# Performance work log

Measured on AMD Instinct MI355X. Metric: run time of the kernel, lower is better.

The kernel has to match this reference:

```python
import jax, jax.numpy as jnp
import numpy as np

BITS = 8
B, S, E = 8, 512, 1024
H = 16
MLP = 4096
LN_EPS = 1e-5


def ste_round(x):
    # straight-through rounding (brevitas round_ste)
    return x + jax.lax.stop_gradient(jnp.round(x) - x)


def fq(x, bits=BITS, signed=True, narrow=False):
    """Per-tensor fake-quant: scale from abs-max stats, round+clamp+rescale."""
    if signed:
        qmax = 2.0 ** (bits - 1) - 1.0
        qmin = -qmax if narrow else -(qmax + 1.0)
        amax = jnp.max(jnp.abs(x))
    else:
        qmax = 2.0 ** bits - 1.0
        qmin = 0.0
        amax = jnp.max(x)
    scale = jnp.maximum(jax.lax.stop_gradient(amax) / qmax, 1e-8)
    return jnp.clip(ste_round(x / scale), qmin, qmax) * scale


def fq_w(w):
    # weight quantizer: 8-bit signed narrow-range, max-stats scale
    return fq(w, bits=8, signed=True, narrow=True)


def layernorm(x, g, b):
    mu = jnp.mean(x, axis=-1, keepdims=True)
    var = jnp.mean(jnp.square(x - mu), axis=-1, keepdims=True)
    return (x - mu) * jax.lax.rsqrt(var + LN_EPS) * g + b


def block_forward(x, Wq, bq, Wk, bk, Wv, bv, Wo, bo, W1, b1, W2, b2, g1, be1, g2, be2):
    Bb, Ss, Ee = x.shape
    D = Ee // H
    # --- quant multihead attention (unpacked in_proj) ---
    q = x @ fq_w(Wq).T + fq(bq, 8)
    k = x @ fq_w(Wk).T + fq(bk, 8)
    v = x @ fq_w(Wv).T + fq(bv, 8)
    qh = q.reshape(Bb, Ss, H, D).transpose(0, 2, 1, 3)   # bhsd
    kh = k.reshape(Bb, Ss, H, D).transpose(0, 2, 1, 3)
    vh = v.reshape(Bb, Ss, H, D).transpose(0, 2, 1, 3)
    q_scaled = fq(qh / jnp.sqrt(jnp.float32(D)))          # q_scaled_quant
    kt = fq(kh)                                            # k_transposed_quant (per-tensor)
    vq = fq(vh)                                            # v_quant
    scores = jnp.einsum('bhqd,bhkd->bhqk', q_scaled, kt)
    scores = fq(scores)                                    # softmax_input_quant
    attn = jax.nn.softmax(scores, axis=-1)
    attn = fq(attn)                                        # attn_output_weights_quant
    ctx = jnp.einsum('bhqk,bhkd->bhqd', attn, vq)
    ctx = ctx.transpose(0, 2, 1, 3).reshape(Bb, Ss, Ee)
    ctx = fq(ctx)                                          # out_proj_input_quant
    sdp_out = ctx @ fq_w(Wo).T + fq(bo, 8)
    # --- residual + norm ---
    h = fq(x) + fq(sdp_out)                                # QuantEltwiseAdd input_quant
    h = fq(layernorm(h, g1, be1))                          # norm_sdp + QuantIdentity
    # --- quant MLP ---
    m = h @ fq_w(W1).T + fq(b1, 8)
    m = fq(jax.nn.relu(m), signed=False)                   # QuantReLU (unsigned)
    m = m @ fq_w(W2).T + fq(b2, 8)
    # --- residual + norm ---
    y = fq(h) + fq(m)
    return fq(layernorm(y, g2, be2))


def setup_inputs() -> dict:
    key = jax.random.key(0)
    ks = jax.random.split(key, 16)
    s_in = 1.0 / np.sqrt(E)
    s_mlp = 1.0 / np.sqrt(MLP)
    return {
        'x': jax.random.normal(ks[0], (B, S, E), jnp.float32),
        'Wq': jax.random.normal(ks[1], (E, E), jnp.float32) * s_in,
        'bq': jax.random.normal(ks[2], (E,), jnp.float32) * 0.01,
        'Wk': jax.random.normal(ks[3], (E, E), jnp.float32) * s_in,
        'bk': jax.random.normal(ks[4], (E,), jnp.float32) * 0.01,
        'Wv': jax.random.normal(ks[5], (E, E), jnp.float32) * s_in,
        'bv': jax.random.normal(ks[6], (E,), jnp.float32) * 0.01,
        'Wo': jax.random.normal(ks[7], (E, E), jnp.float32) * s_in,
        'bo': jax.random.normal(ks[8], (E,), jnp.float32) * 0.01,
        'W1': jax.random.normal(ks[9], (MLP, E), jnp.float32) * s_in,
        'b1': jax.random.normal(ks[10], (MLP,), jnp.float32) * 0.01,
        'W2': jax.random.normal(ks[11], (E, MLP), jnp.float32) * s_mlp,
        'b2': jax.random.normal(ks[12], (E,), jnp.float32) * 0.01,
        'g1': jnp.ones((E,), jnp.float32),
        'be1': jnp.zeros((E,), jnp.float32),
        'g2': jnp.ones((E,), jnp.float32),
        'be2': jnp.zeros((E,), jnp.float32),
    }


def reference(x, Wq, bq, Wk, bk, Wv, bv, Wo, bo, W1, b1, W2, b2, g1, be1, g2, be2):
    return block_forward(x, Wq, bq, Wk, bk, Wv, bv, Wo, bo, W1, b1, W2, b2, g1, be1, g2, be2)
```

## Files before the change

kernel.cpp:

```cpp
#include <hip/hip_runtime.h>
#include <math.h>

#define BB 8
#define SS 512
#define EE 1024
#define HH 16
#define DD 64
#define MLPD 4096
#define NROWS (BB*SS)
#define LNEPS 1e-5f
#define SM_ROWS 8
#define LN_ROWS 8

typedef unsigned short u16;
typedef __attribute__((ext_vector_type(8))) short bf8_t;
typedef __attribute__((ext_vector_type(4))) float f32x4;

enum {
  SL_WQ=0, SL_WK, SL_WV, SL_WO, SL_W1, SL_W2,
  SL_BQ, SL_BK, SL_BV, SL_BO, SL_B1, SL_B2,
  SL_X, SL_Q, SL_K, SL_V, SL_SC, SL_AT, SL_CTX, SL_SDP,
  SL_LN1, SL_M1, SL_M2, SL_LN2, NSLOTS
};

__device__ __forceinline__ void atomicMaxF(float* a, float v) {
  atomicMax((unsigned int*)a, __float_as_uint(v));
}

__device__ __forceinline__ float fqv(float x, float inv, float s, float lo, float hi) {
  return fminf(fmaxf(rintf(x * inv), lo), hi) * s;
}

__device__ __forceinline__ u16 f2bf(float f) {
  unsigned int u = __float_as_uint(f);
  return (u16)((u + 0x7fffu + ((u >> 16) & 1u)) >> 16);
}
__device__ __forceinline__ float bf2f(u16 h) {
  return __uint_as_float((unsigned int)h << 16);
}

__device__ __forceinline__ void gll16(const void* src, void* dst) {
  __builtin_amdgcn_global_load_lds((const __attribute__((address_space(1))) void*)src,
                                   (__attribute__((address_space(3))) void*)dst, 16, 0, 0);
}

__global__ void k_init(float* scal) {
  if (threadIdx.x < NSLOTS) scal[threadIdx.x] = 0.f;
}

__global__ __launch_bounds__(256) void k_amax(const float* __restrict__ p, int n,
                                              float* scal, int slot) {
  float m = 0.f;
  for (int i = blockIdx.x * 256 + threadIdx.x; i < n; i += gridDim.x * 256)
    m = fmaxf(m, fabsf(p[i]));
  #pragma unroll
  for (int o = 32; o > 0; o >>= 1) m = fmaxf(m, __shfl_down(m, o, 64));
  __shared__ float red[4];
  int w = threadIdx.x >> 6;
  if ((threadIdx.x & 63) == 0) red[w] = m;
  __syncthreads();
  if (threadIdx.x == 0) {
    m = fmaxf(fmaxf(red[0], red[1]), fmaxf(red[2], red[3]));
    atomicMaxF(&scal[slot], m);
  }
}

__global__ __launch_bounds__(256) void k_conv_code(const float* __restrict__ in,
    u16* __restrict__ out, long n, const float* __restrict__ scal, int slot,
    float div, float lo, float hi)
{
  const float s = fmaxf(scal[slot] / div, 1e-8f), inv = 1.f / s;
  long i = ((long)blockIdx.x * 256 + threadIdx.x) * 4;
  const long stride = (long)gridDim.x * 1024;
  for (; i < n; i += stride) {
    const float4 v = *(const float4*)&in[i];
    ushort4 o;
    o.x = f2bf(fminf(fmaxf(rintf(v.x * inv), lo), hi));
    o.y = f2bf(fminf(fmaxf(rintf(v.y * inv), lo), hi));
    o.z = f2bf(fminf(fmaxf(rintf(v.z * inv), lo), hi));
    o.w = f2bf(fminf(fmaxf(rintf(v.w * inv), lo), hi));
    *(ushort4*)&out[i] = o;
  }
}

__global__ __launch_bounds__(256) void k_conv_x(const float* __restrict__ in,
    u16* __restrict__ hi, u16* __restrict__ lo, long n)
{
  long i = ((long)blockIdx.x * 256 + threadIdx.x) * 4;
  const long stride = (long)gridDim.x * 1024;
  for (; i < n; i += stride) {
    const float4 v = *(const float4*)&in[i];
    ushort4 h, l;
    h.x = f2bf(v.x); l.x = f2bf(v.x - bf2f(h.x));
    h.y = f2bf(v.y); l.y = f2bf(v.y - bf2f(h.y));
    h.z = f2bf(v.z); l.z = f2bf(v.z - bf2f(h.z));
    h.w = f2bf(v.w); l.w = f2bf(v.w - bf2f(h.w));
    *(ushort4*)&hi[i] = h;
    *(ushort4*)&lo[i] = l;
  }
}

template<bool RAWX>
__global__ __launch_bounds__(256) void k_gemm_mfma(
    const u16* __restrict__ A0, const u16* __restrict__ A1,
    const u16* __restrict__ Bw, const float* __restrict__ bias,
    float* __restrict__ C, int M, int N, int K,
    const float* __restrict__ scal, float* scalw,
    int aslot, float adiv, int bslot, int biasslot, int epi, int epislot)
{
  __shared__ u16 As[128*32];
  __shared__ u16 Al[RAWX ? 128*32 : 16];
  __shared__ u16 Bs[128*32];
  __shared__ float red[4];

  const int t = threadIdx.x;
  const int w = t >> 6, lane = t & 63;
  const int wr = w >> 1, wc = w & 1;
  const int lr = lane & 15, cbl = lane >> 4;
  const int swz = (lr >> 1) & 3;
  const int m0 = blockIdx.y * 128, n0 = blockIdx.x * 128;

  const int srow0 = t >> 2;
  const int scb   = (t & 3) ^ ((srow0 >> 1) & 3);
  const int lo0 = w * 512;
  const int lo1 = 2048 + w * 512;
  const long arow0 = (long)(m0 + srow0)      * K + scb * 8;
  const long arow1 = (long)(m0 + srow0 + 64) * K + scb * 8;
  const long brow0 = (long)(n0 + srow0)      * K + scb * 8;
  const long brow1 = (long)(n0 + srow0 + 64) * K + scb * 8;

  int afo[4], bfo[4];
  #pragma unroll
  for (int i = 0; i < 4; ++i) {
    afo[i] = (wr*64 + i*16 + lr) * 32 + ((cbl ^ swz) * 8);
    bfo[i] = (wc*64 + i*16 + lr) * 32 + ((cbl ^ swz) * 8);
  }

  f32x4 acc[4][4] = {};

  for (int k0 = 0; k0 < K; k0 += 32) {
    gll16(A0 + arow0 + k0, As + lo0);
    gll16(A0 + arow1 + k0, As + lo1);
    if (RAWX) {
      gll16(A1 + arow0 + k0, Al + lo0);
      gll16(A1 + arow1 + k0, Al + lo1);
    }
    gll16(Bw + brow0 + k0, Bs + lo0);
    gll16(Bw + brow1 + k0, Bs + lo1);
    __syncthreads();

    bf8_t afr[4], bfr[4], alo[4];
    #pragma unroll
    for (int i = 0; i < 4; ++i) {
      afr[i] = *(const bf8_t*)&As[afo[i]];
      bfr[i] = *(const bf8_t*)&Bs[bfo[i]];
      if (RAWX) alo[i] = *(const bf8_t*)&Al[afo[i]];
    }
    #pragma unroll
    for (int i = 0; i < 4; ++i)
      #pragma unroll
      for (int j = 0; j < 4; ++j) {
        acc[i][j] = __builtin_amdgcn_mfma_f32_16x16x32_bf16(afr[i], bfr[j], acc[i][j], 0, 0, 0);
        if (RAWX)
          acc[i][j] = __builtin_amdgcn_mfma_f32_16x16x32_bf16(alo[i], bfr[j], acc[i][j], 0, 0, 0);
      }
    __syncthreads();
  }

  float sA = 1.f;
  if (aslot >= 0) sA = fmaxf(scal[aslot] / adiv, 1e-8f);
  const float sB = fmaxf(scal[bslot] / 127.f, 1e-8f);
  const float sAB = sA * sB;
  const float sb = fmaxf(scal[biasslot] / 127.f, 1e-8f), invb = 1.f / sb;

  float em = 0.f;
  #pragma unroll
  for (int j = 0; j < 4; ++j) {
    const int col = n0 + wc*64 + j*16 + lr;
    const float bq = fqv(bias[col], invb, sb, -128.f, 127.f);
    #pragma unroll
    for (int i = 0; i < 4; ++i) {
      const int rowb = m0 + wr*64 + i*16 + cbl*4;
      #pragma unroll
      for (int r = 0; r < 4; ++r) {
        const float c = acc[i][j][r] * sAB + bq;
        C[(long)(rowb + r) * N + col] = c;
        em = (epi == 2) ? fmaxf(em, c) : fmaxf(em, fabsf(c));
      }
    }
  }
  #pragma unroll
  for (int o = 32; o > 0; o >>= 1) em = fmaxf(em, __shfl_down(em, o, 64));
  if ((lane) == 0) red[w] = em;
  __syncthreads();
  if (t == 0)
    atomicMaxF(&scalw[epislot], fmaxf(fmaxf(red[0], red[1]), fmaxf(red[2], red[3])));
}

__global__ __launch_bounds__(256) void k_scores(
    const float* __restrict__ q, const float* __restrict__ kk,
    float* __restrict__ sc, float* scal)
{
  __shared__ float Qs[64][65];
  __shared__ float Ks[64][65];
  __shared__ float red[4];
  const int bz = blockIdx.z, b = bz >> 4, h = bz & 15;
  const int tx = threadIdx.x & 15, ty = threadIdx.x >> 4;
  const int m0 = blockIdx.y * 64, n0 = blockIdx.x * 64;
  const long base = (long)b * SS * EE + h * DD;

  const float sq = fmaxf((scal[SL_Q] * 0.125f) / 127.f, 1e-8f), invq = 1.f / sq;
  const float sk = fmaxf(scal[SL_K] / 127.f, 1e-8f), invk = 1.f / sk;

  #pragma unroll
  for (int p = 0; p < 16; ++p) {
    int e = threadIdx.x + p * 256;
    int r = e >> 6, c = e & 63;
    float qv = q[base + (long)(m0 + r) * EE + c] * 0.125f;
    Qs[c][r] = fqv(qv, invq, sq, -128.f, 127.f);
    float kv = kk[base + (long)(n0 + r) * EE + c];
    Ks[c][r] = fqv(kv, invk, sk, -128.f, 127.f);
  }
  __syncthreads();

  float acc[4][4] = {{0.f}};
  #pragma unroll
  for (int kx = 0; kx < 64; ++kx) {
    float a[4], bv[4];
    #pragma unroll
    for (int i = 0; i < 4; ++i) a[i] = Qs[kx][ty + 16 * i];
    #pragma unroll
    for (int j = 0; j < 4; ++j) bv[j] = Ks[kx][tx + 16 * j];
    #pragma unroll
    for (int i = 0; i < 4; ++i)
      #pragma unroll
      for (int j = 0; j < 4; ++j)
        acc[i][j] += a[i] * bv[j];
  }

  float em = 0.f;
  #pragma unroll
  for (int i = 0; i < 4; ++i)
    #pragma unroll
    for (int j = 0; j < 4; ++j) {
      float c = acc[i][j];
      sc[((long)bz * SS + m0 + ty + 16 * i) * SS + n0 + tx + 16 * j] = c;
      em = fmaxf(em, fabsf(c));
    }
  #pragma unroll
  for (int o = 32; o > 0; o >>= 1) em = fmaxf(em, __shfl_down(em, o, 64));
  int w = threadIdx.x >> 6;
  if ((threadIdx.x & 63) == 0) red[w] = em;
  __syncthreads();
  if (threadIdx.x == 0)
    atomicMaxF(&scal[SL_SC], fmaxf(fmaxf(red[0], red[1]), fmaxf(red[2], red[3])));
}

__global__ __launch_bounds__(256) void k_softmax(float* __restrict__ sc, float* scal) {
  const int w = threadIdx.x >> 6, lane = threadIdx.x & 63;
  const float ss = fmaxf(scal[SL_SC] / 127.f, 1e-8f), inv = 1.f / ss;
  float am = 0.f;
  long row = ((long)blockIdx.x * 4 + w) * SM_ROWS;
  for (int r = 0; r < SM_ROWS; ++r, ++row) {
    float4* p = (float4*)(sc + row * SS);
    float4 a = p[lane];
    float4 b = p[lane + 64];
    float v[8];
    v[0] = fqv(a.x, inv, ss, -128.f, 127.f);
    v[1] = fqv(a.y, inv, ss, -128.f, 127.f);
    v[2] = fqv(a.z, inv, ss, -128.f, 127.f);
    v[3] = fqv(a.w, inv, ss, -128.f, 127.f);
    v[4] = fqv(b.x, inv, ss, -128.f, 127.f);
    v[5] = fqv(b.y, inv, ss, -128.f, 127.f);
    v[6] = fqv(b.z, inv, ss, -128.f, 127.f);
    v[7] = fqv(b.w, inv, ss, -128.f, 127.f);
    float m = v[0];
    #pragma unroll
    for (int i = 1; i < 8; ++i) m = fmaxf(m, v[i]);
    #pragma unroll
    for (int o = 32; o > 0; o >>= 1) m = fmaxf(m, __shfl_xor(m, o, 64));
    float e[8], s = 0.f;
    #pragma unroll
    for (int i = 0; i < 8; ++i) { e[i] = expf(v[i] - m); s += e[i]; }
    #pragma unroll
    for (int o = 32; o > 0; o >>= 1) s += __shfl_xor(s, o, 64);
    const float rinv = 1.f / s;
    a.x = e[0] * rinv; a.y = e[1] * rinv; a.z = e[2] * rinv; a.w = e[3] * rinv;
    b.x = e[4] * rinv; b.y = e[5] * rinv; b.z = e[6] * rinv; b.w = e[7] * rinv;
    p[lane] = a;
    p[lane + 64] = b;
    am = fmaxf(am, rinv);
  }
  __shared__ float red[4];
  if (lane == 0) red[w] = am;
  __syncthreads();
  if (threadIdx.x == 0)
    atomicMaxF(&scal[SL_AT], fmaxf(fmaxf(red[0], red[1]), fmaxf(red[2], red[3])));
}

__global__ __launch_bounds__(256) void k_ctx(
    const float* __restrict__ at, const float* __restrict__ v,
    float* __restrict__ ctx, float* scal)
{
  __shared__ float As[16][65];
  __shared__ float Vs[16][68];
  __shared__ float red[4];
  const int bz = blockIdx.y, b = bz >> 4, h = bz & 15;
  const int tx = threadIdx.x & 15, ty = threadIdx.x >> 4;
  const int m0 = blockIdx.x * 64;
  const long abase = (long)bz * SS * SS;
  const long vbase = (long)b * SS * EE + h * DD;

  const float sa = fmaxf(scal[SL_AT] / 127.f, 1e-8f), inva = 1.f / sa;
  const float sv = fmaxf(scal[SL_V] / 127.f, 1e-8f), invv = 1.f / sv;

  float acc[4][4] = {{0.f}};
  for (int k0 = 0; k0 < SS; k0 += 16) {
    #pragma unroll
    for (int p = 0; p < 4; ++p) {
      int e = threadIdx.x + p * 256;
      int r = e >> 4, c = e & 15;
      float a = at[abase + (long)(m0 + r) * SS + k0 + c];
      As[c][r] = fqv(a, inva, sa, -128.f, 127.f);
    }
    {
      int r = threadIdx.x >> 6, c = threadIdx.x & 63;
      #pragma unroll
      for (int p = 0; p < 4; ++p) {
        int rr = r + p * 4;
        float vv = v[vbase + (long)(k0 + rr) * EE + c];
        Vs[rr][c] = fqv(vv, invv, sv, -128.f, 127.f);
      }
    }
    __syncthreads();
    #pragma unroll
    for (int kx = 0; kx < 16; ++kx) {
      float a[4], bv[4];
      #pragma unroll
      for (int i = 0; i < 4; ++i) a[i] = As[kx][ty + 16 * i];
      #pragma unroll
      for (int j = 0; j < 4; ++j) bv[j] = Vs[kx][tx + 16 * j];
      #pragma unroll
      for (int i = 0; i < 4; ++i)
        #pragma unroll
        for (int j = 0; j < 4; ++j)
          acc[i][j] += a[i] * bv[j];
    }
    __syncthreads();
  }

  float em = 0.f;
  #pragma unroll
  for (int i = 0; i < 4; ++i)
    #pragma unroll
    for (int j = 0; j < 4; ++j) {
      float c = acc[i][j];
      ctx[((long)b * SS + m0 + ty + 16 * i) * EE + h * DD + tx + 16 * j] = c;
      em = fmaxf(em, fabsf(c));
    }
  #pragma unroll
  for (int o = 32; o > 0; o >>= 1) em = fmaxf(em, __shfl_down(em, o, 64));
  int w = threadIdx.x >> 6;
  if ((threadIdx.x & 63) == 0) red[w] = em;
  __syncthreads();
  if (threadIdx.x == 0)
    atomicMaxF(&scal[SL_CTX], fmaxf(fmaxf(red[0], red[1]), fmaxf(red[2], red[3])));
}

__global__ __launch_bounds__(256) void k_ln(
    const float* __restrict__ A, const float* __restrict__ Bt,
    const float* __restrict__ g, const float* __restrict__ be,
    float* __restrict__ out, float* scal, int slotA, int slotB, int oslot)
{
  const float sa = fmaxf(scal[slotA] / 127.f, 1e-8f), ia = 1.f / sa;
  const float sb = fmaxf(scal[slotB] / 127.f, 1e-8f), ib = 1.f / sb;

  __shared__ float red[4];
  const int w = threadIdx.x >> 6;
  float em = 0.f;

  for (int rr = 0; rr < LN_ROWS; ++rr) {
    const long base = ((long)blockIdx.x * LN_ROWS + rr) * EE;
    float v[4];
    float sum = 0.f;
    #pragma unroll
    for (int p = 0; p < 4; ++p) {
      int c = threadIdx.x + p * 256;
      float av = fqv(A[base + c], ia, sa, -128.f, 127.f);
      float bv = fqv(Bt[base + c], ib, sb, -128.f, 127.f);
      v[p] = av + bv;
      sum += v[p];
    }
    #pragma unroll
    for (int o = 32; o > 0; o >>= 1) sum += __shfl_down(sum, o, 64);
    if ((threadIdx.x & 63) == 0) red[w] = sum;
    __syncthreads();
    const float mu = (red[0] + red[1] + red[2] + red[3]) * (1.f / EE);
    __syncthreads();

    float vs = 0.f;
    #pragma unroll
    for (int p = 0; p < 4; ++p) { float d = v[p] - mu; vs += d * d; }
    #pragma unroll
    for (int o = 32; o > 0; o >>= 1) vs += __shfl_down(vs, o, 64);
    if ((threadIdx.x & 63) == 0) red[w] = vs;
    __syncthreads();
    const float var = (red[0] + red[1] + red[2] + red[3]) * (1.f / EE);
    const float rs = 1.f / sqrtf(var + LNEPS);
    __syncthreads();

    #pragma unroll
    for (int p = 0; p < 4; ++p) {
      int c = threadIdx.x + p * 256;
      float o = (v[p] - mu) * rs * g[c] + be[c];
      out[base + c] = o;
      em = fmaxf(em, fabsf(o));
    }
  }

  #pragma unroll
  for (int o = 32; o > 0; o >>= 1) em = fmaxf(em, __shfl_down(em, o, 64));
  if ((threadIdx.x & 63) == 0) red[w] = em;
  __syncthreads();
  if (threadIdx.x == 0)
    atomicMaxF(&scal[oslot], fmaxf(fmaxf(red[0], red[1]), fmaxf(red[2], red[3])));
}

__global__ __launch_bounds__(256) void k_fq_out(float* __restrict__ o, float* scal) {
  const float s = fmaxf(scal[SL_LN2] / 127.f, 1e-8f), inv = 1.f / s;
  #pragma unroll
  for (int p = 0; p < 4; ++p) {
    long idx = (long)blockIdx.x * 1024 + threadIdx.x + p * 256;
    o[idx] = fqv(o[idx], inv, s, -128.f, 127.f);
  }
}

extern "C" void kernel_launch(void* const* d_in, const int* in_sizes, int n_in,
                              void* d_out, int out_size, void* d_ws, size_t ws_size,
                              hipStream_t stream) {
  (void)in_sizes; (void)n_in; (void)out_size; (void)ws_size;
  const float* x   = (const float*)d_in[0];
  const float* Wq  = (const float*)d_in[1];
  const float* bq  = (const float*)d_in[2];
  const float* Wk  = (const float*)d_in[3];
  const float* bk  = (const float*)d_in[4];
  const float* Wv  = (const float*)d_in[5];
  const float* bv  = (const float*)d_in[6];
  const float* Wo  = (const float*)d_in[7];
  const float* bo  = (const float*)d_in[8];
  const float* W1  = (const float*)d_in[9];
  const float* b1  = (const float*)d_in[10];
  const float* W2  = (const float*)d_in[11];
  const float* b2  = (const float*)d_in[12];
  const float* g1  = (const float*)d_in[13];
  const float* be1 = (const float*)d_in[14];
  const float* g2  = (const float*)d_in[15];
  const float* be2 = (const float*)d_in[16];
  float* out = (float*)d_out;

  char* W = (char*)d_ws;
  const long MB = 1024 * 1024;
  float* scal = (float*)W;
  u16* wqc  = (u16*)(W + 1*MB);
  u16* wkc  = (u16*)(W + 3*MB);
  u16* wvc  = (u16*)(W + 5*MB);
  u16* woc  = (u16*)(W + 7*MB);
  float* qb = (float*)(W + 16*MB);
  float* kb = (float*)(W + 32*MB);
  float* vb = (float*)(W + 48*MB);
  float* sc = (float*)(W + 64*MB);
  u16* xhi  = (u16*)(W + 64*MB);
  u16* xlo  = (u16*)(W + 72*MB);
  u16* ctxq = (u16*)(W + 64*MB);
  u16* w1c  = (u16*)(W + 72*MB);
  u16* w2c  = (u16*)(W + 80*MB);
  u16* ln1q = (u16*)(W + 88*MB);
  float* m1 = (float*)(W + 96*MB);
  u16* m1q  = (u16*)(W + 160*MB);
  float* m2 = kb;

  k_init<<<dim3(1), dim3(64), 0, stream>>>(scal);

  auto AM = [&](const float* p, long n, int slot) {
    int blocks = (int)((n + 255) / 256);
    if (blocks > 256) blocks = 256;
    k_amax<<<dim3(blocks), dim3(256), 0, stream>>>(p, (int)n, scal, slot);
  };
  AM(Wq, (long)EE*EE, SL_WQ); AM(Wk, (long)EE*EE, SL_WK);
  AM(Wv, (long)EE*EE, SL_WV); AM(Wo, (long)EE*EE, SL_WO);
  AM(W1, (long)MLPD*EE, SL_W1); AM(W2, (long)MLPD*EE, SL_W2);
  AM(bq, EE, SL_BQ); AM(bk, EE, SL_BK); AM(bv, EE, SL_BV); AM(bo, EE, SL_BO);
  AM(b1, MLPD, SL_B1); AM(b2, EE, SL_B2);
  AM(x, (long)NROWS*EE, SL_X);

  auto CONV = [&](const float* in, u16* o, long n, int slot, float div, float lo, float hi) {
    int blocks = (int)(n / 1024);
    if (blocks > 2048) blocks = 2048;
    k_conv_code<<<dim3(blocks), dim3(256), 0, stream>>>(in, o, n, scal, slot, div, lo, hi);
  };

  CONV(Wq, wqc, (long)EE*EE, SL_WQ, 127.f, -127.f, 127.f);
  CONV(Wk, wkc, (long)EE*EE, SL_WK, 127.f, -127.f, 127.f);
  CONV(Wv, wvc, (long)EE*EE, SL_WV, 127.f, -127.f, 127.f);
  CONV(Wo, woc, (long)EE*EE, SL_WO, 127.f, -127.f, 127.f);
  k_conv_x<<<dim3(2048), dim3(256), 0, stream>>>(x, xhi, xlo, (long)NROWS*EE);

  const dim3 blk(256);
  const dim3 gp(EE/128, NROWS/128);
  const dim3 gm1(MLPD/128, NROWS/128);

  k_gemm_mfma<true><<<gp, blk, 0, stream>>>(xhi, xlo, wqc, bq, qb, NROWS, EE, EE,
      scal, scal, -1, 1.f, SL_WQ, SL_BQ, 1, SL_Q);
  k_gemm_mfma<true><<<gp, blk, 0, stream>>>(xhi, xlo, wkc, bk, kb, NROWS, EE, EE,
      scal, scal, -1, 1.f, SL_WK, SL_BK, 1, SL_K);
  k_gemm_mfma<true><<<gp, blk, 0, stream>>>(xhi, xlo, wvc, bv, vb, NROWS, EE, EE,
      scal, scal, -1, 1.f, SL_WV, SL_BV, 1, SL_V);

  k_scores<<<dim3(SS/64, SS/64, BB*HH), blk, 0, stream>>>(qb, kb, sc, scal);
  k_softmax<<<dim3(BB*HH*SS/(4*SM_ROWS)), blk, 0, stream>>>(sc, scal);
  k_ctx<<<dim3(SS/64, BB*HH), blk, 0, stream>>>(sc, vb, qb, scal);

  CONV(qb, ctxq, (long)NROWS*EE, SL_CTX, 127.f, -128.f, 127.f);
  CONV(W1, w1c, (long)MLPD*EE, SL_W1, 127.f, -127.f, 127.f);
  CONV(W2, w2c, (long)MLPD*EE, SL_W2, 127.f, -127.f, 127.f);
  k_gemm_mfma<false><<<gp, blk, 0, stream>>>(ctxq, ctxq, woc, bo, kb, NROWS, EE, EE,
      scal, scal, SL_CTX, 127.f, SL_WO, SL_BO, 1, SL_SDP);

  k_ln<<<dim3(NROWS/LN_ROWS), blk, 0, stream>>>(x, kb, g1, be1, vb, scal, SL_X, SL_SDP, SL_LN1);

  CONV(vb, ln1q, (long)NROWS*EE, SL_LN1, 127.f, -128.f, 127.f);
  k_gemm_mfma<false><<<gm1, blk, 0, stream>>>(ln1q, ln1q, w1c, b1, m1, NROWS, MLPD, EE,
      scal, scal, SL_LN1, 127.f, SL_W1, SL_B1, 2, SL_M1);

  CONV(m1, m1q, (long)NROWS*MLPD, SL_M1, 255.f, 0.f, 255.f);
  k_gemm_mfma<false><<<gp, blk, 0, stream>>>(m1q, m1q, w2c, b2, m2, NROWS, EE, MLPD,
      scal, scal, SL_M1, 255.f, SL_W2, SL_B2, 1, SL_M2);

  k_ln<<<dim3(NROWS/LN_ROWS), blk, 0, stream>>>(vb, m2, g2, be2, out, scal, SL_LN1, SL_M2, SL_LN2);
  k_fq_out<<<dim3(NROWS), blk, 0, stream>>>(out, scal);
}
```

Baseline: 902.2 us.

## Move attention score and context matmuls to bf16 MFMA with pre-quantized Q/K/V

Replaces the FP32 scalar-FMA scores and context kernels with MFMA bf16 kernels. Q and K are pre-quantized to integer codes stored as bf16, and V is quantized and transposed per head so it can be loaded like a GEMM operand. The per-tensor scales are applied in the epilogue. The workspace layout is reshuffled to hold the new code buffers. This adds three conversion passes and extra memory traffic in exchange for matrix-core throughput on the two attention matmuls.

```diff
diff --git a/kernel.cpp b/kernel.cpp
--- a/kernel.cpp
+++ b/kernel.cpp
@@ -67,9 +67,9 @@
 
 __global__ __launch_bounds__(256) void k_conv_code(const float* __restrict__ in,
     u16* __restrict__ out, long n, const float* __restrict__ scal, int slot,
-    float div, float lo, float hi)
+    float div, float smul, float lo, float hi)
 {
-  const float s = fmaxf(scal[slot] / div, 1e-8f), inv = 1.f / s;
+  const float s = fmaxf(scal[slot] / div, 1e-8f) * smul, inv = 1.f / s;
   long i = ((long)blockIdx.x * 256 + threadIdx.x) * 4;
   const long stride = (long)gridDim.x * 1024;
   for (; i < n; i += stride) {
@@ -100,6 +100,41 @@
   }
 }
 
+__global__ __launch_bounds__(256) void k_conv_vt(
+    const float* __restrict__ v, u16* __restrict__ vt, const float* __restrict__ scal)
+{
+  __shared__ u16 Ls[64][72];
+  const int t = threadIdx.x;
+  const int bz = blockIdx.y, b = bz >> 4, h = bz & 15;
+  const int s0 = blockIdx.x * 64;
+  const float sv = fmaxf(scal[SL_V] / 127.f, 1e-8f), inv = 1.f / sv;
+
+  const int sl = t >> 2, c4 = t & 3;
+  const long src = ((long)b * SS + s0 + sl) * EE + h * DD + c4 * 16;
+  #pragma unroll
+  for (int u = 0; u < 4; ++u) {
+    const float4 x4 = *(const float4*)&v[src + u * 4];
+    ushort4 o;
+    o.x = f2bf(fminf(fmaxf(rintf(x4.x * inv), -128.f), 127.f));
+    o.y = f2bf(fminf(fmaxf(rintf(x4.y * inv), -128.f), 127.f));
+    o.z = f2bf(fminf(fmaxf(rintf(x4.z * inv), -128.f), 127.f));
+    o.w = f2bf(fminf(fmaxf(rintf(x4.w * inv), -128.f), 127.f));
+    *(ushort4*)&Ls[sl][c4 * 16 + u * 4] = o;
+  }
+  __syncthreads();
+  const int d = t >> 2, sg = t & 3;
+  const long dst = ((long)bz * DD + d) * SS + s0 + sg * 16;
+  #pragma unroll
+  for (int u = 0; u < 4; ++u) {
+    ushort4 o;
+    o.x = Ls[sg * 16 + u * 4 + 0][d];
+    o.y = Ls[sg * 16 + u * 4 + 1][d];
+    o.z = Ls[sg * 16 + u * 4 + 2][d];
+    o.w = Ls[sg * 16 + u * 4 + 3][d];
+    *(ushort4*)&vt[dst + u * 4] = o;
+  }
+}
+
 template<bool RAWX>
 __global__ __launch_bounds__(256) void k_gemm_mfma(
     const u16* __restrict__ A0, const u16* __restrict__ A1,
@@ -191,68 +226,92 @@
   }
   #pragma unroll
   for (int o = 32; o > 0; o >>= 1) em = fmaxf(em, __shfl_down(em, o, 64));
-  if ((lane) == 0) red[w] = em;
+  if (lane == 0) red[w] = em;
   __syncthreads();
   if (t == 0)
     atomicMaxF(&scalw[epislot], fmaxf(fmaxf(red[0], red[1]), fmaxf(red[2], red[3])));
 }
 
-__global__ __launch_bounds__(256) void k_scores(
-    const float* __restrict__ q, const float* __restrict__ kk,
+__global__ __launch_bounds__(256) void k_scores_mfma(
+    const u16* __restrict__ qc, const u16* __restrict__ kc,
     float* __restrict__ sc, float* scal)
 {
-  __shared__ float Qs[64][65];
-  __shared__ float Ks[64][65];
+  __shared__ u16 As[128*32];
+  __shared__ u16 Bs[128*32];
   __shared__ float red[4];
-  const int bz = blockIdx.z, b = bz >> 4, h = bz & 15;
-  const int tx = threadIdx.x & 15, ty = threadIdx.x >> 4;
-  const int m0 = blockIdx.y * 64, n0 = blockIdx.x * 64;
-  const long base = (long)b * SS * EE + h * DD;
-
-  const float sq = fmaxf((scal[SL_Q] * 0.125f) / 127.f, 1e-8f), invq = 1.f / sq;
-  const float sk = fmaxf(scal[SL_K] / 127.f, 1e-8f), invk = 1.f / sk;
-
-  #pragma unroll
-  for (int p = 0; p < 16; ++p) {
-    int e = threadIdx.x + p * 256;
-    int r = e >> 6, c = e & 63;
-    float qv = q[base + (long)(m0 + r) * EE + c] * 0.125f;
-    Qs[c][r] = fqv(qv, invq, sq, -128.f, 127.f);
-    float kv = kk[base + (long)(n0 + r) * EE + c];
-    Ks[c][r] = fqv(kv, invk, sk, -128.f, 127.f);
-  }
-  __syncthreads();
-
-  float acc[4][4] = {{0.f}};
-  #pragma unroll
-  for (int kx = 0; kx < 64; ++kx) {
-    float a[4], bv[4];
-    #pragma unroll
-    for (int i = 0; i < 4; ++i) a[i] = Qs[kx][ty + 16 * i];
-    #pragma unroll
-    for (int j = 0; j < 4; ++j) bv[j] = Ks[kx][tx + 16 * j];
+
+  const int t = threadIdx.x;
+  const int w = t >> 6, lane = t & 63;
+  const int wr = w >> 1, wc = w & 1;
+  const int lr = lane & 15, cbl = lane >> 4;
+  const int swz = (lr >> 1) & 3;
+  const int bz = blockIdx.z;
+  const int m0 = blockIdx.y * 128, n0 = blockIdx.x * 128;
+  const long base = (long)(bz >> 4) * SS * EE + (bz & 15) * DD;
+
+  const int srow0 = t >> 2;
+  const int scb   = (t & 3) ^ ((srow0 >> 1) & 3);
+  const int lo0 = w * 512;
+  const int lo1 = 2048 + w * 512;
+  const long ar0 = base + (long)(m0 + srow0)      * EE + scb * 8;
+  const long ar1 = base + (long)(m0 + srow0 + 64) * EE + scb * 8;
+  const long br0 = base + (long)(n0 + srow0)      * EE + scb * 8;
+  const long br1 = base + (long)(n0 + srow0 + 64) * EE + scb * 8;
+
+  int afo[4], bfo[4];
+  #pragma unroll
+  for (int i = 0; i < 4; ++i) {
+    afo[i] = (wr*64 + i*16 + lr) * 32 + ((cbl ^ swz) * 8);
+    bfo[i] = (wc*64 + i*16 + lr) * 32 + ((cbl ^ swz) * 8);
+  }
+
+  f32x4 acc[4][4] = {};
+
+  for (int k0 = 0; k0 < DD; k0 += 32) {
+    gll16(qc + ar0 + k0, As + lo0);
+    gll16(qc + ar1 + k0, As + lo1);
+    gll16(kc + br0 + k0, Bs + lo0);
+    gll16(kc + br1 + k0, Bs + lo1);
+    __syncthreads();
+
+    bf8_t afr[4], bfr[4];
+    #pragma unroll
+    for (int i = 0; i < 4; ++i) {
+      afr[i] = *(const bf8_t*)&As[afo[i]];
+      bfr[i] = *(const bf8_t*)&Bs[bfo[i]];
+    }
     #pragma unroll
     for (int i = 0; i < 4; ++i)
       #pragma unroll
       for (int j = 0; j < 4; ++j)
-        acc[i][j] += a[i] * bv[j];
-  }
+        acc[i][j] = __builtin_amdgcn_mfma_f32_16x16x32_bf16(afr[i], bfr[j], acc[i][j], 0, 0, 0);
+    __syncthreads();
+  }
+
+  const float sq = fmaxf(scal[SL_Q] / 1016.f, 1e-8f);
+  const float sk = fmaxf(scal[SL_K] / 127.f, 1e-8f);
+  const float sqk = sq * sk;
 
   float em = 0.f;
   #pragma unroll
-  for (int i = 0; i < 4; ++i)
-    #pragma unroll
-    for (int j = 0; j < 4; ++j) {
-      float c = acc[i][j];
-      sc[((long)bz * SS + m0 + ty + 16 * i) * SS + n0 + tx + 16 * j] = c;
-      em = fmaxf(em, fabsf(c));
-    }
+  for (int j = 0; j < 4; ++j) {
+    const int col = n0 + wc*64 + j*16 + lr;
+    #pragma unroll
+    for (int i = 0; i < 4; ++i) {
+      const int rowb = m0 + wr*64 + i*16 + cbl*4;
+      #pragma unroll
+      for (int r = 0; r < 4; ++r) {
+        const float c = acc[i][j][r] * sqk;
+        sc[(long)bz * SS * SS + (long)(rowb + r) * SS + col] = c;
+        em = fmaxf(em, fabsf(c));
+      }
+    }
+  }
   #pragma unroll
   for (int o = 32; o > 0; o >>= 1) em = fmaxf(em, __shfl_down(em, o, 64));
-  int w = threadIdx.x >> 6;
-  if ((threadIdx.x & 63) == 0) red[w] = em;
+  if (lane == 0) red[w] = em;
   __syncthreads();
-  if (threadIdx.x == 0)
+  if (t == 0)
     atomicMaxF(&scal[SL_SC], fmaxf(fmaxf(red[0], red[1]), fmaxf(red[2], red[3])));
 }
 
@@ -298,72 +357,92 @@
     atomicMaxF(&scal[SL_AT], fmaxf(fmaxf(red[0], red[1]), fmaxf(red[2], red[3])));
 }
 
-__global__ __launch_bounds__(256) void k_ctx(
-    const float* __restrict__ at, const float* __restrict__ v,
+__global__ __launch_bounds__(256) void k_ctx_mfma(
+    const float* __restrict__ at, const u16* __restrict__ vt,
     float* __restrict__ ctx, float* scal)
 {
-  __shared__ float As[16][65];
-  __shared__ float Vs[16][68];
+  __shared__ u16 As[128*32];
+  __shared__ u16 Bs[64*32];
   __shared__ float red[4];
+
+  const int t = threadIdx.x;
+  const int w = t >> 6, lane = t & 63;
+  const int wr = w >> 1, wc = w & 1;
+  const int lr = lane & 15, cbl = lane >> 4;
+  const int swz = (lr >> 1) & 3;
   const int bz = blockIdx.y, b = bz >> 4, h = bz & 15;
-  const int tx = threadIdx.x & 15, ty = threadIdx.x >> 4;
-  const int m0 = blockIdx.x * 64;
+  const int m0 = blockIdx.x * 128;
   const long abase = (long)bz * SS * SS;
-  const long vbase = (long)b * SS * EE + h * DD;
+  const long vtbase = (long)bz * DD * SS;
 
   const float sa = fmaxf(scal[SL_AT] / 127.f, 1e-8f), inva = 1.f / sa;
-  const float sv = fmaxf(scal[SL_V] / 127.f, 1e-8f), invv = 1.f / sv;
-
-  float acc[4][4] = {{0.f}};
-  for (int k0 = 0; k0 < SS; k0 += 16) {
-    #pragma unroll
-    for (int p = 0; p < 4; ++p) {
-      int e = threadIdx.x + p * 256;
-      int r = e >> 4, c = e & 15;
-      float a = at[abase + (long)(m0 + r) * SS + k0 + c];
-      As[c][r] = fqv(a, inva, sa, -128.f, 127.f);
-    }
-    {
-      int r = threadIdx.x >> 6, c = threadIdx.x & 63;
+  const float sv = fmaxf(scal[SL_V] / 127.f, 1e-8f);
+
+  const int bsrow = t >> 2;
+  const int bscb  = (t & 3) ^ ((bsrow >> 1) & 3);
+  const long bsrc = vtbase + (long)bsrow * SS + bscb * 8;
+
+  int afo[4], bfo[2];
+  #pragma unroll
+  for (int i = 0; i < 4; ++i)
+    afo[i] = (wr*64 + i*16 + lr) * 32 + ((cbl ^ swz) * 8);
+  #pragma unroll
+  for (int j = 0; j < 2; ++j)
+    bfo[j] = (wc*32 + j*16 + lr) * 32 + ((cbl ^ swz) * 8);
+
+  f32x4 acc[4][2] = {};
+
+  for (int k0 = 0; k0 < SS; k0 += 32) {
+    gll16(vt + bsrc + k0, Bs + w * 512);
+    #pragma unroll
+    for (int i = 0; i < 4; ++i) {
+      const int s = i * 256 + t;
+      const int row = s >> 3, c4 = s & 7;
+      const float4 v4 = *(const float4*)&at[abase + (long)(m0 + row) * SS + k0 + c4 * 4];
+      ushort4 o;
+      o.x = f2bf(fminf(fmaxf(rintf(v4.x * inva), -128.f), 127.f));
+      o.y = f2bf(fminf(fmaxf(rintf(v4.y * inva), -128.f), 127.f));
+      o.z = f2bf(fminf(fmaxf(rintf(v4.z * inva), -128.f), 127.f));
+      o.w = f2bf(fminf(fmaxf(rintf(v4.w * inva), -128.f), 127.f));
+      const int off = row * 32 + (((c4 >> 1) ^ ((row >> 1) & 3)) * 8) + (c4 & 1) * 4;
+      *(ushort4*)&As[off] = o;
+    }
+    __syncthreads();
+
+    bf8_t afr[4], bfr[2];
+    #pragma unroll
+    for (int i = 0; i < 4; ++i) afr[i] = *(const bf8_t*)&As[afo[i]];
+    #pragma unroll
+    for (int j = 0; j < 2; ++j) bfr[j] = *(const bf8_t*)&Bs[bfo[j]];
+    #pragma unroll
+    for (int i = 0; i < 4; ++i)
       #pragma unroll
-      for (int p = 0; p < 4; ++p) {
-        int rr = r + p * 4;
-        float vv = v[vbase + (long)(k0 + rr) * EE + c];
-        Vs[rr][c] = fqv(vv, invv, sv, -128.f, 127.f);
+      for (int j = 0; j < 2; ++j)
+        acc[i][j] = __builtin_amdgcn_mfma_f32_16x16x32_bf16(afr[i], bfr[j], acc[i][j], 0, 0, 0);
+    __syncthreads();
+  }
+
+  const float sav = sa * sv;
+  float em = 0.f;
+  #pragma unroll
+  for (int j = 0; j < 2; ++j) {
+    const int col = h * DD + wc*32 + j*16 + lr;
+    #pragma unroll
+    for (int i = 0; i < 4; ++i) {
+      const int rowb = m0 + wr*64 + i*16 + cbl*4;
+      #pragma unroll
+      for (int r = 0; r < 4; ++r) {
+        const float c = acc[i][j][r] * sav;
+        ctx[((long)b * SS + rowb + r) * EE + col] = c;
+        em = fmaxf(em, fabsf(c));
       }
     }
-    __syncthreads();
-    #pragma unroll
-    for (int kx = 0; kx < 16; ++kx) {
-      float a[4], bv[4];
-      #pragma unroll
-      for (int i = 0; i < 4; ++i) a[i] = As[kx][ty + 16 * i];
-      #pragma unroll
-      for (int j = 0; j < 4; ++j) bv[j] = Vs[kx][tx + 16 * j];
-      #pragma unroll
-      for (int i = 0; i < 4; ++i)
-        #pragma unroll
-        for (int j = 0; j < 4; ++j)
-          acc[i][j] += a[i] * bv[j];
-    }
-    __syncthreads();
-  }
-
-  float em = 0.f;
-  #pragma unroll
-  for (int i = 0; i < 4; ++i)
-    #pragma unroll
-    for (int j = 0; j < 4; ++j) {
-      float c = acc[i][j];
-      ctx[((long)b * SS + m0 + ty + 16 * i) * EE + h * DD + tx + 16 * j] = c;
-      em = fmaxf(em, fabsf(c));
-    }
+  }
   #pragma unroll
   for (int o = 32; o > 0; o >>= 1) em = fmaxf(em, __shfl_down(em, o, 64));
-  int w = threadIdx.x >> 6;
-  if ((threadIdx.x & 63) == 0) red[w] = em;
+  if (lane == 0) red[w] = em;
   __syncthreads();
-  if (threadIdx.x == 0)
+  if (t == 0)
     atomicMaxF(&scal[SL_CTX], fmaxf(fmaxf(red[0], red[1]), fmaxf(red[2], red[3])));
 }
 
@@ -465,19 +544,25 @@
   u16* wkc  = (u16*)(W + 3*MB);
   u16* wvc  = (u16*)(W + 5*MB);
   u16* woc  = (u16*)(W + 7*MB);
-  float* qb = (float*)(W + 16*MB);
-  float* kb = (float*)(W + 32*MB);
-  float* vb = (float*)(W + 48*MB);
-  float* sc = (float*)(W + 64*MB);
-  u16* xhi  = (u16*)(W + 64*MB);
-  u16* xlo  = (u16*)(W + 72*MB);
-  u16* ctxq = (u16*)(W + 64*MB);
-  u16* w1c  = (u16*)(W + 72*MB);
-  u16* w2c  = (u16*)(W + 80*MB);
-  u16* ln1q = (u16*)(W + 88*MB);
-  float* m1 = (float*)(W + 96*MB);
-  u16* m1q  = (u16*)(W + 160*MB);
-  float* m2 = kb;
+  u16* xhi  = (u16*)(W + 16*MB);
+  u16* xlo  = (u16*)(W + 24*MB);
+  float* qb = (float*)(W + 48*MB);
+  float* kb = (float*)(W + 64*MB);
+  float* vb = (float*)(W + 80*MB);
+  u16* qc   = (u16*)(W + 144*MB);
+  u16* kc   = (u16*)(W + 152*MB);
+  u16* vt   = (u16*)(W + 160*MB);
+  float* sc = (float*)(W + 16*MB);
+  float* ctxb = (float*)(W + 168*MB);
+  u16* ctxq = (u16*)(W + 144*MB);
+  float* sdp = (float*)(W + 16*MB);
+  float* ln1 = (float*)(W + 32*MB);
+  u16* ln1q = (u16*)(W + 48*MB);
+  u16* w1c  = (u16*)(W + 56*MB);
+  u16* w2c  = (u16*)(W + 64*MB);
+  float* m1 = (float*)(W + 72*MB);
+  u16* m1q  = (u16*)(W + 136*MB);
+  float* m2 = (float*)(W + 168*MB);
 
   k_init<<<dim3(1), dim3(64), 0, stream>>>(scal);
 
@@ -493,16 +578,17 @@
   AM(b1, MLPD, SL_B1); AM(b2, EE, SL_B2);
   AM(x, (long)NROWS*EE, SL_X);
 
-  auto CONV = [&](const float* in, u16* o, long n, int slot, float div, float lo, float hi) {
+  auto CONV = [&](const float* in, u16* o, long n, int slot, float div, float smul,
+                  float lo, float hi) {
     int blocks = (int)(n / 1024);
     if (blocks > 2048) blocks = 2048;
-    k_conv_code<<<dim3(blocks), dim3(256), 0, stream>>>(in, o, n, scal, slot, div, lo, hi);
+    k_conv_code<<<dim3(blocks), dim3(256), 0, stream>>>(in, o, n, scal, slot, div, smul, lo, hi);
   };
 
-  CONV(Wq, wqc, (long)EE*EE, SL_WQ, 127.f, -127.f, 127.f);
-  CONV(Wk, wkc, (long)EE*EE, SL_WK, 127.f, -127.f, 127.f);
-  CONV(Wv, wvc, (long)EE*EE, SL_WV, 127.f, -127.f, 127.f);
-  CONV(Wo, woc, (long)EE*EE, SL_WO, 127.f, -127.f, 127.f);
+  CONV(Wq, wqc, (long)EE*EE, SL_WQ, 127.f, 1.f, -127.f, 127.f);
+  CONV(Wk, wkc, (long)EE*EE, SL_WK, 127.f, 1.f, -127.f, 127.f);
+  CONV(Wv, wvc, (long)EE*EE, SL_WV, 127.f, 1.f, -127.f, 127.f);
+  CONV(Wo, woc, (long)EE*EE, SL_WO, 127.f, 1.f, -127.f, 127.f);
   k_conv_x<<<dim3(2048), dim3(256), 0, stream>>>(x, xhi, xlo, (long)NROWS*EE);
 
   const dim3 blk(256);
@@ -516,26 +602,30 @@
   k_gemm_mfma<true><<<gp, blk, 0, stream>>>(xhi, xlo, wvc, bv, vb, NROWS, EE, EE,
       scal, scal, -1, 1.f, SL_WV, SL_BV, 1, SL_V);
 
-  k_scores<<<dim3(SS/64, SS/64, BB*HH), blk, 0, stream>>>(qb, kb, sc, scal);
+  CONV(qb, qc, (long)NROWS*EE, SL_Q, 1016.f, 8.f, -128.f, 127.f);
+  CONV(kb, kc, (long)NROWS*EE, SL_K, 127.f, 1.f, -128.f, 127.f);
+  k_conv_vt<<<dim3(SS/64, BB*HH), blk, 0, stream>>>(vb, vt, scal);
+
+  k_scores_mfma<<<dim3(SS/128, SS/128, BB*HH), blk, 0, stream>>>(qc, kc, sc, scal);
   k_softmax<<<dim3(BB*HH*SS/(4*SM_ROWS)), blk, 0, stream>>>(sc, scal);
-  k_ctx<<<dim3(SS/64, BB*HH), blk, 0, stream>>>(sc, vb, qb, scal);
-
-  CONV(qb, ctxq, (long)NROWS*EE, SL_CTX, 127.f, -128.f, 127.f);
-  CONV(W1, w1c, (long)MLPD*EE, SL_W1, 127.f, -127.f, 127.f);
-  CONV(W2, w2c, (long)MLPD*EE, SL_W2, 127.f, -127.f, 127.f);
-  k_gemm_mfma<false><<<gp, blk, 0, stream>>>(ctxq, ctxq, woc, bo, kb, NROWS, EE, EE,
+  k_ctx_mfma<<<dim3(SS/128, BB*HH), blk, 0, stream>>>(sc, vt, ctxb, scal);
+
+  CONV(ctxb, ctxq, (long)NROWS*EE, SL_CTX, 127.f, 1.f, -128.f, 127.f);
+  CONV(W1, w1c, (long)MLPD*EE, SL_W1, 127.f, 1.f, -127.f, 127.f);
+  CONV(W2, w2c, (long)MLPD*EE, SL_W2, 127.f, 1.f, -127.f, 127.f);
+  k_gemm_mfma<false><<<gp, blk, 0, stream>>>(ctxq, ctxq, woc, bo, sdp, NROWS, EE, EE,
       scal, scal, SL_CTX, 127.f, SL_WO, SL_BO, 1, SL_SDP);
 
-  k_ln<<<dim3(NROWS/LN_ROWS), blk, 0, stream>>>(x, kb, g1, be1, vb, scal, SL_X, SL_SDP, SL_LN1);
-
-  CONV(vb, ln1q, (long)NROWS*EE, SL_LN1, 127.f, -128.f, 127.f);
+  k_ln<<<dim3(NROWS/LN_ROWS), blk, 0, stream>>>(x, sdp, g1, be1, ln1, scal, SL_X, SL_SDP, SL_LN1);
+
+  CONV(ln1, ln1q, (long)NROWS*EE, SL_LN1, 127.f, 1.f, -128.f, 127.f);
   k_gemm_mfma<false><<<gm1, blk, 0, stream>>>(ln1q, ln1q, w1c, b1, m1, NROWS, MLPD, EE,
       scal, scal, SL_LN1, 127.f, SL_W1, SL_B1, 2, SL_M1);
 
-  CONV(m1, m1q, (long)NROWS*MLPD, SL_M1, 255.f, 0.f, 255.f);
+  CONV(m1, m1q, (long)NROWS*MLPD, SL_M1, 255.f, 1.f, 0.f, 255.f);
   k_gemm_mfma<false><<<gp, blk, 0, stream>>>(m1q, m1q, w2c, b2, m2, NROWS, EE, MLPD,
       scal, scal, SL_M1, 255.f, SL_W2, SL_B2, 1, SL_M2);
 
-  k_ln<<<dim3(NROWS/LN_ROWS), blk, 0, stream>>>(vb, m2, g2, be2, out, scal, SL_LN1, SL_M2, SL_LN2);
+  k_ln<<<dim3(NROWS/LN_ROWS), blk, 0, stream>>>(ln1, m2, g2, be2, out, scal, SL_LN1, SL_M2, SL_LN2);
   k_fq_out<<<dim3(NROWS), blk, 0, stream>>>(out, scal);
 }
```

Result: faster. 837.7 us (-7.1%).
